# Kernel optimization log

Hardware: AMD Instinct MI355X
Metric: run time of the kernel (lower is better)

## Reference

```python
import jax, jax.numpy as jnp
import numpy as np

B, S, L, F = 32, 48, 64, 256


def setup_inputs() -> dict:
    key = jax.random.key(0)
    ks = jax.random.split(key, 7)
    return {
        "features": jax.random.normal(ks[0], (B, S, L, F), dtype=jnp.float32),
        "src_locs": jax.random.normal(ks[1], (B, L, 2), dtype=jnp.float32),
        "tar_locs": jax.random.normal(ks[2], (B, 2), dtype=jnp.float32),
        "W1": jax.random.normal(ks[3], (F, F), dtype=jnp.float32) * (1.0 / np.sqrt(F)),
        "b1": jax.random.normal(ks[4], (F,), dtype=jnp.float32) * 0.02,
        "W2": jax.random.normal(ks[5], (F, 1), dtype=jnp.float32) * (1.0 / np.sqrt(F)),
        "b2": jax.random.normal(ks[6], (1,), dtype=jnp.float32) * 0.02,
    }


def reference(features, src_locs, tar_locs, W1, b1, W2, b2):
    # features: (B, S, L, F); src_locs: (B, L, 2); tar_locs: (B, 2)
    # MLP score: Linear(F,F) + ReLU + Linear(F,1) + ReLU -> (B, S, L, 1)
    attn = jax.nn.relu(jnp.einsum('bslf,fg->bslg', features, W1) + b1)
    attn = jax.nn.relu(jnp.einsum('bslf,fo->bslo', attn, W2) + b2)  # (B,S,L,1)
    # inverse-distance weights over stations: (B, L)
    dists = jnp.sqrt(jnp.sum((src_locs - tar_locs[:, None, :]) ** 2, axis=-1))
    inv_dists = 1.0 / dists  # (B, L)
    # broadcast to (B, 1, L, 1), softmax over src_length axis (axis=2)
    attn_scores = jax.nn.softmax(attn * inv_dists[:, None, :, None], axis=2)
    # weighted sum over stations -> (B, S, F)
    return jnp.sum(features * attn_scores, axis=2)
```

## Files before the change

kernel.cpp:

```cpp
#include <hip/hip_runtime.h>
#include <hip/hip_fp16.h>
#include <math.h>

typedef _Float16 half8 __attribute__((ext_vector_type(8)));
typedef float floatx4 __attribute__((ext_vector_type(4)));

#define BB 32
#define SS 48
#define LL 64
#define FF 256

__global__ __launch_bounds__(256) void prep_w(const float* __restrict__ W1,
                                              _Float16* __restrict__ whi,
                                              _Float16* __restrict__ wlo) {
    int idx = blockIdx.x * 256 + threadIdx.x;
    int j    = idx & 7;
    int lane = (idx >> 3) & 63;
    int nt   = (idx >> 9) & 15;
    int kt   = idx >> 13;
    int k = kt * 32 + ((lane >> 4) & 3) * 8 + j;
    int n = nt * 16 + (lane & 15);
    float x = W1[k * FF + n];
    _Float16 hi = (_Float16)x;
    _Float16 lo = (_Float16)(x - (float)hi);
    whi[idx] = hi;
    wlo[idx] = lo;
}

__global__ __launch_bounds__(256, 3) void ida_mfma(
    const float* __restrict__ features,
    const float* __restrict__ src_locs,
    const float* __restrict__ tar_locs,
    const _Float16* __restrict__ whi,
    const _Float16* __restrict__ wlo,
    const float* __restrict__ b1,
    const float* __restrict__ W2,
    const float* __restrict__ b2,
    float* __restrict__ out)
{
    __shared__ float SP[LL * 4];
    __shared__ float wbuf[LL];
    __shared__ float red[4 * FF];

    const int t    = threadIdx.x;
    const int w    = t >> 6;
    const int lane = t & 63;
    const int quad = lane >> 4;
    const int l16  = lane & 15;
    const int bs   = blockIdx.x;
    const int b    = bs / SS;

    const float* Xg = features + (size_t)bs * (LL * FF);

    floatx4 acc[4][4] = {};

    #pragma unroll
    for (int kt = 0; kt < 8; ++kt) {
        half8 bhi[4], blo[4];
        #pragma unroll
        for (int nt = 0; nt < 4; ++nt) {
            size_t off = ((size_t)(kt * 16 + (w * 4 + nt)) * 64 + lane) * 8;
            bhi[nt] = *((const half8*)(whi + off));
            blo[nt] = *((const half8*)(wlo + off));
        }
        #pragma unroll
        for (int mt = 0; mt < 4; ++mt) {
            const float4* p = (const float4*)(Xg + (mt * 16 + l16) * FF + kt * 32 + quad * 8);
            float4 x0 = p[0], x1 = p[1];
            float xs[8] = {x0.x, x0.y, x0.z, x0.w, x1.x, x1.y, x1.z, x1.w};
            half8 ahi, alo;
            #pragma unroll
            for (int j = 0; j < 8; ++j) {
                _Float16 h = (_Float16)xs[j];
                ahi[j] = h;
                alo[j] = (_Float16)(xs[j] - (float)h);
            }
            #pragma unroll
            for (int nt = 0; nt < 4; ++nt) {
                acc[mt][nt] = __builtin_amdgcn_mfma_f32_16x16x32_f16(ahi, bhi[nt], acc[mt][nt], 0, 0, 0);
                acc[mt][nt] = __builtin_amdgcn_mfma_f32_16x16x32_f16(ahi, blo[nt], acc[mt][nt], 0, 0, 0);
                acc[mt][nt] = __builtin_amdgcn_mfma_f32_16x16x32_f16(alo, bhi[nt], acc[mt][nt], 0, 0, 0);
            }
        }
    }

    float b1v[4], w2v[4];
    #pragma unroll
    for (int nt = 0; nt < 4; ++nt) {
        int n = (w * 4 + nt) * 16 + l16;
        b1v[nt] = b1[n];
        w2v[nt] = W2[n];
    }
    #pragma unroll
    for (int mt = 0; mt < 4; ++mt) {
        #pragma unroll
        for (int r = 0; r < 4; ++r) {
            float p = 0.f;
            #pragma unroll
            for (int nt = 0; nt < 4; ++nt) {
                float h = fmaxf(acc[mt][nt][r] + b1v[nt], 0.f);
                p = fmaf(h, w2v[nt], p);
            }
            p += __shfl_xor(p, 1);
            p += __shfl_xor(p, 2);
            p += __shfl_xor(p, 4);
            p += __shfl_xor(p, 8);
            if (l16 == 0) SP[(mt * 16 + quad * 4 + r) * 4 + w] = p;
        }
    }
    __syncthreads();

    if (t < LL) {
        float s = SP[4 * t] + SP[4 * t + 1] + SP[4 * t + 2] + SP[4 * t + 3] + b2[0];
        float score = fmaxf(s, 0.f);
        float dx = src_locs[(b * LL + t) * 2 + 0] - tar_locs[b * 2 + 0];
        float dy = src_locs[(b * LL + t) * 2 + 1] - tar_locs[b * 2 + 1];
        float inv = 1.0f / sqrtf(dx * dx + dy * dy);
        float logit = score * inv;
        float m = logit;
        #pragma unroll
        for (int o = 32; o > 0; o >>= 1) m = fmaxf(m, __shfl_xor(m, o));
        float e = __expf(logit - m);
        float se = e;
        #pragma unroll
        for (int o = 32; o > 0; o >>= 1) se += __shfl_xor(se, o);
        wbuf[t] = e / se;
    }
    __syncthreads();

    {
        const float4* Xg4 = (const float4*)Xg;
        floatx4 o = {0.f, 0.f, 0.f, 0.f};
        #pragma unroll
        for (int lr = 0; lr < 16; ++lr) {
            int l = w * 16 + lr;
            float wl = wbuf[l];
            float4 x = Xg4[l * 64 + lane];
            o[0] = fmaf(x.x, wl, o[0]);
            o[1] = fmaf(x.y, wl, o[1]);
            o[2] = fmaf(x.z, wl, o[2]);
            o[3] = fmaf(x.w, wl, o[3]);
        }
        #pragma unroll
        for (int j = 0; j < 4; ++j)
            red[w * FF + lane * 4 + j] = o[j];
    }
    __syncthreads();
    {
        float o = red[0 * FF + t] + red[1 * FF + t] + red[2 * FF + t] + red[3 * FF + t];
        out[bs * FF + t] = o;
    }
}

extern "C" void kernel_launch(void* const* d_in, const int* in_sizes, int n_in,
                              void* d_out, int out_size, void* d_ws, size_t ws_size,
                              hipStream_t stream) {
    const float* features = (const float*)d_in[0];
    const float* src_locs = (const float*)d_in[1];
    const float* tar_locs = (const float*)d_in[2];
    const float* W1       = (const float*)d_in[3];
    const float* b1       = (const float*)d_in[4];
    const float* W2       = (const float*)d_in[5];
    const float* b2       = (const float*)d_in[6];
    float* out = (float*)d_out;

    _Float16* whi = (_Float16*)d_ws;
    _Float16* wlo = whi + FF * FF;

    prep_w<<<dim3(FF * FF / 256), dim3(256), 0, stream>>>(W1, whi, wlo);
    ida_mfma<<<dim3(BB * SS), dim3(256), 0, stream>>>(
        features, src_locs, tar_locs, whi, wlo, b1, W2, b2, out);
}
```

Before: 201.2 us.

## Stage hi/lo split of features in LDS and hold W1 fragments in registers

Before, every wave loaded and split all 64 rows of features to fp16 hi/lo on its own, so each block did that conversion four times over. Now each wave converts only its 16 rows and writes the hi/lo fragments to shared memory, where all waves read them for the MFMAs. W1 fragments for half of K are held in registers and the second half is prefetched after the first half's MFMAs. This cuts redundant global loads and conversions, but it adds barriers, 32KB of LDS and more registers, and the occupancy target drops from 3 to 2.

```diff
diff --git a/kernel.cpp b/kernel.cpp
--- a/kernel.cpp
+++ b/kernel.cpp
@@ -27,7 +27,7 @@
     wlo[idx] = lo;
 }
 
-__global__ __launch_bounds__(256, 3) void ida_mfma(
+__global__ __launch_bounds__(256, 2) void ida_mfma(
     const float* __restrict__ features,
     const float* __restrict__ src_locs,
     const float* __restrict__ tar_locs,
@@ -38,6 +38,8 @@
     const float* __restrict__ b2,
     float* __restrict__ out)
 {
+    __shared__ _Float16 Ahi[8192];
+    __shared__ _Float16 Alo[8192];
     __shared__ float SP[LL * 4];
     __shared__ float wbuf[LL];
     __shared__ float red[4 * FF];
@@ -53,34 +55,60 @@
     const float* Xg = features + (size_t)bs * (LL * FF);
 
     floatx4 acc[4][4] = {};
+    half8 bh[4][4], bl[4][4];
 
     #pragma unroll
-    for (int kt = 0; kt < 8; ++kt) {
-        half8 bhi[4], blo[4];
+    for (int ktl = 0; ktl < 4; ++ktl)
         #pragma unroll
         for (int nt = 0; nt < 4; ++nt) {
-            size_t off = ((size_t)(kt * 16 + (w * 4 + nt)) * 64 + lane) * 8;
-            bhi[nt] = *((const half8*)(whi + off));
-            blo[nt] = *((const half8*)(wlo + off));
-        }
-        #pragma unroll
-        for (int mt = 0; mt < 4; ++mt) {
-            const float4* p = (const float4*)(Xg + (mt * 16 + l16) * FF + kt * 32 + quad * 8);
+            size_t off = ((size_t)(ktl * 16 + w * 4 + nt) * 64 + lane) * 8;
+            bh[ktl][nt] = *((const half8*)(whi + off));
+            bl[ktl][nt] = *((const half8*)(wlo + off));
+        }
+
+    for (int kh = 0; kh < 2; ++kh) {
+        __syncthreads();
+        for (int ktl = 0; ktl < 4; ++ktl) {
+            int kt = kh * 4 + ktl;
+            const float4* p = (const float4*)(Xg + (w * 16 + l16) * FF + kt * 32 + quad * 8);
             float4 x0 = p[0], x1 = p[1];
             float xs[8] = {x0.x, x0.y, x0.z, x0.w, x1.x, x1.y, x1.z, x1.w};
-            half8 ahi, alo;
+            half8 hi, lo;
             #pragma unroll
             for (int j = 0; j < 8; ++j) {
                 _Float16 h = (_Float16)xs[j];
-                ahi[j] = h;
-                alo[j] = (_Float16)(xs[j] - (float)h);
+                hi[j] = h;
+                lo[j] = (_Float16)(xs[j] - (float)h);
             }
-            #pragma unroll
-            for (int nt = 0; nt < 4; ++nt) {
-                acc[mt][nt] = __builtin_amdgcn_mfma_f32_16x16x32_f16(ahi, bhi[nt], acc[mt][nt], 0, 0, 0);
-                acc[mt][nt] = __builtin_amdgcn_mfma_f32_16x16x32_f16(ahi, blo[nt], acc[mt][nt], 0, 0, 0);
-                acc[mt][nt] = __builtin_amdgcn_mfma_f32_16x16x32_f16(alo, bhi[nt], acc[mt][nt], 0, 0, 0);
+            *((half8*)&Ahi[((w * 4 + ktl) * 64 + lane) * 8]) = hi;
+            *((half8*)&Alo[((w * 4 + ktl) * 64 + lane) * 8]) = lo;
+        }
+        __syncthreads();
+
+        #pragma unroll
+        for (int ktl = 0; ktl < 4; ++ktl) {
+            #pragma unroll
+            for (int mt = 0; mt < 4; ++mt) {
+                half8 ahi = *((half8*)&Ahi[((mt * 4 + ktl) * 64 + lane) * 8]);
+                half8 alo = *((half8*)&Alo[((mt * 4 + ktl) * 64 + lane) * 8]);
+                #pragma unroll
+                for (int nt = 0; nt < 4; ++nt) {
+                    acc[mt][nt] = __builtin_amdgcn_mfma_f32_16x16x32_f16(ahi, bh[ktl][nt], acc[mt][nt], 0, 0, 0);
+                    acc[mt][nt] = __builtin_amdgcn_mfma_f32_16x16x32_f16(ahi, bl[ktl][nt], acc[mt][nt], 0, 0, 0);
+                    acc[mt][nt] = __builtin_amdgcn_mfma_f32_16x16x32_f16(alo, bh[ktl][nt], acc[mt][nt], 0, 0, 0);
+                }
             }
+        }
+
+        if (kh == 0) {
+            #pragma unroll
+            for (int ktl = 0; ktl < 4; ++ktl)
+                #pragma unroll
+                for (int nt = 0; nt < 4; ++nt) {
+                    size_t off = ((size_t)((4 + ktl) * 16 + w * 4 + nt) * 64 + lane) * 8;
+                    bh[ktl][nt] = *((const half8*)(whi + off));
+                    bl[ktl][nt] = *((const half8*)(wlo + off));
+                }
         }
     }
 
```

Measured after the change: 182.6 us. 9.2% less time.
